# Optimization experiments

Measured on AMD Instinct MI355X. Metric: run time of the kernel, lower is better.

The kernel has to match this reference:

```python
import jax, jax.numpy as jnp
import numpy as np

B, S, D, H = 2, 2048, 1024, 16
DH = D // H
SCALE = 1.0 / float(np.sqrt(DH))


def setup_inputs() -> dict:
    key = jax.random.key(0)
    ks = jax.random.split(key, 5)
    x = jax.random.normal(ks[0], (B, S, D), dtype=jnp.float32)
    init = 0.02
    Wq = jax.random.normal(ks[1], (D, D), dtype=jnp.float32) * init
    Wk = jax.random.normal(ks[2], (D, D), dtype=jnp.float32) * init
    Wv = jax.random.normal(ks[3], (D, D), dtype=jnp.float32) * init
    Wo = jax.random.normal(ks[4], (D, D), dtype=jnp.float32) * init
    bq = jnp.zeros((D,), dtype=jnp.float32)
    bk = jnp.zeros((D,), dtype=jnp.float32)
    bv = jnp.zeros((D,), dtype=jnp.float32)
    bo = jnp.zeros((D,), dtype=jnp.float32)
    return {"x": x, "Wq": Wq, "bq": bq, "Wk": Wk, "bk": bk,
            "Wv": Wv, "bv": bv, "Wo": Wo, "bo": bo}


def reference(x, Wq, bq, Wk, bk, Wv, bv, Wo, bo):
    # torch Linear: y = x @ W.T + b  (W: [out, in])
    q = x @ Wq.T + bq  # [B,S,D]
    k = x @ Wk.T + bk
    v = x @ Wv.T + bv
    # split heads -> [B,H,S,dh]
    q = q.reshape(B, S, H, DH).transpose(0, 2, 1, 3)
    k = k.reshape(B, S, H, DH).transpose(0, 2, 1, 3)
    v = v.reshape(B, S, H, DH).transpose(0, 2, 1, 3)
    scores = jnp.einsum('bhqd,bhkd->bhqk', q, k) * SCALE  # [B,H,S,S]
    p = jax.nn.softmax(scores, axis=-1)
    o = jnp.einsum('bhqk,bhkd->bhqd', p, v)  # [B,H,S,dh]
    # faithful to original: view(B, d_model, S) then transpose(-1,-2)
    o = o.reshape(B, D, S).swapaxes(-1, -2)  # [B,S,D]
    return o @ Wo.T + bo
```

## Files before the change

kernel.cpp:

```cpp
#include <hip/hip_runtime.h>
#include <cstdint>
#include <cstddef>


typedef _Float16 h16;
typedef _Float16 h16x8 __attribute__((ext_vector_type(8)));
typedef _Float16 h16x4 __attribute__((ext_vector_type(4)));
typedef float    f32x4 __attribute__((ext_vector_type(4)));
typedef unsigned int u32x4 __attribute__((ext_vector_type(4)));

#define MFMA16 __builtin_amdgcn_mfma_f32_16x16x32_f16

#define QSCALE 0.1803368801111204f

#if __has_builtin(__builtin_amdgcn_exp2f)
#define EXP2F(x) __builtin_amdgcn_exp2f(x)
#else
#define EXP2F(x) exp2f(x)
#endif

__device__ __forceinline__ void gload_lds16(char* lds_dst, const void* gsrc) {
  __builtin_amdgcn_global_load_lds(
      (__attribute__((address_space(1))) void*)gsrc,
      (__attribute__((address_space(3))) void*)lds_dst,
      16, 0, 0);
}

__device__ __forceinline__ unsigned pk2(float lo, float hi) {
  return __builtin_bit_cast(unsigned, __builtin_amdgcn_cvt_pkrtz(lo, hi));
}

__device__ __forceinline__ void swap32(unsigned& a, unsigned& b) {
  asm("v_permlane32_swap_b32 %0, %1" : "+v"(a), "+v"(b));
}

__device__ __forceinline__ h16x8 mk8(unsigned u0, unsigned u1, unsigned u2, unsigned u3) {
  u32x4 v = {u0, u1, u2, u3};
  return __builtin_bit_cast(h16x8, v);
}


__global__ __launch_bounds__(256)
void cast_all(const float* __restrict__ x,
              const float* __restrict__ wq, const float* __restrict__ wk,
              const float* __restrict__ wv, const float* __restrict__ wo,
              h16* __restrict__ xb, h16* __restrict__ wqb, h16* __restrict__ wkb,
              h16* __restrict__ wvb, h16* __restrict__ wob) {
  const int z = blockIdx.y;
  const float* src; h16* dst; int n4;
  switch (z) {
    case 0:  src = x;  dst = xb;  n4 = 1048576; break;
    case 1:  src = wq; dst = wqb; n4 = 262144;  break;
    case 2:  src = wk; dst = wkb; n4 = 262144;  break;
    case 3:  src = wv; dst = wvb; n4 = 262144;  break;
    default: src = wo; dst = wob; n4 = 262144;  break;
  }
  int i = blockIdx.x * 256 + threadIdx.x;
  const int stride = gridDim.x * 256;
  for (; i < n4; i += stride) {
    float4 v = reinterpret_cast<const float4*>(src)[i];
    h16x4 o = { (h16)v.x, (h16)v.y, (h16)v.z, (h16)v.w };
    reinterpret_cast<h16x4*>(dst)[i] = o;
  }
}

__device__ __forceinline__ void gemm_core_128(
    const h16* __restrict__ A, const h16* __restrict__ W,
    char* lds, f32x4 (&acc)[4][4])
{
  const int tid  = threadIdx.x;
  const int lane = tid & 63;
  const int w    = tid >> 6;
  const int wr   = w >> 1, wc = w & 1;
  const int blockRow = blockIdx.y * 128;
  const int blockCol = blockIdx.x * 128;

  const int sr  = (tid >> 2) & 15;
  const int sc  = tid & 3;
  const int skc = sc ^ ((sr >> 1) & 3);

  const h16* srcA0 = A + (size_t)(blockRow + (0 * 4 + w) * 16 + sr) * 1024 + skc * 8;
  const h16* srcA1 = A + (size_t)(blockRow + (1 * 4 + w) * 16 + sr) * 1024 + skc * 8;
  const h16* srcB0 = W + (size_t)(blockCol + (0 * 4 + w) * 16 + sr) * 1024 + skc * 8;
  const h16* srcB1 = W + (size_t)(blockCol + (1 * 4 + w) * 16 + sr) * 1024 + skc * 8;

  const int dA0o = w * 1024;
  const int dA1o = 4096 + w * 1024;
  const int dB0o = 8192 + w * 1024;
  const int dB1o = 12288 + w * 1024;

  const int fr = lane & 15, fg = lane >> 4;
  const int foff = fr * 64 + ((fg ^ ((fr >> 1) & 3)) << 4);

#pragma unroll
  for (int i = 0; i < 4; ++i)
#pragma unroll
    for (int j = 0; j < 4; ++j) acc[i][j] = f32x4{0.f, 0.f, 0.f, 0.f};

  gload_lds16(lds + dA0o, srcA0);
  gload_lds16(lds + dA1o, srcA1);
  gload_lds16(lds + dB0o, srcB0);
  gload_lds16(lds + dB1o, srcB1);

  for (int ks = 0; ks < 32; ++ks) {
    char* buf = lds + (ks & 1) * 16384;
    __syncthreads();
    if (ks != 31) {
      char* nbuf = lds + ((ks & 1) ^ 1) * 16384;
      gload_lds16(nbuf + dA0o, srcA0 + (ks + 1) * 32);
      gload_lds16(nbuf + dA1o, srcA1 + (ks + 1) * 32);
      gload_lds16(nbuf + dB0o, srcB0 + (ks + 1) * 32);
      gload_lds16(nbuf + dB1o, srcB1 + (ks + 1) * 32);
    }
    char* ldsA = buf;
    char* ldsB = buf + 8192;

    h16x8 af[4], bfv[4];
#pragma unroll
    for (int t = 0; t < 4; ++t)
      af[t] = *(const h16x8*)(ldsA + (wr * 4 + t) * 1024 + foff);
#pragma unroll
    for (int t = 0; t < 4; ++t)
      bfv[t] = *(const h16x8*)(ldsB + (wc * 4 + t) * 1024 + foff);
#pragma unroll
    for (int i = 0; i < 4; ++i)
#pragma unroll
      for (int j = 0; j < 4; ++j)
        acc[i][j] = MFMA16(af[i], bfv[j], acc[i][j], 0, 0, 0);
  }
}

__global__ __launch_bounds__(256, 2)
void gemm_qkv(const h16* __restrict__ xb,
              const h16* __restrict__ wq, const h16* __restrict__ wk, const h16* __restrict__ wv,
              const float* __restrict__ bq, const float* __restrict__ bk, const float* __restrict__ bv,
              h16* __restrict__ q_, h16* __restrict__ k_, h16* __restrict__ vt_)
{
  __shared__ alignas(128) char lds[32768];
  const int z = blockIdx.z;
  const h16* W = (z == 0) ? wq : (z == 1) ? wk : wv;
  const float* bias = (z == 0) ? bq : (z == 1) ? bk : bv;

  f32x4 acc[4][4];
  gemm_core_128(xb, W, lds, acc);

  const int lane = threadIdx.x & 63;
  const int w = threadIdx.x >> 6;
  const int wr = w >> 1, wc = w & 1;
  const int fr = lane & 15, fg = lane >> 4;
  const int blockRow = blockIdx.y * 128;
  const int blockCol = blockIdx.x * 128;

  if (z == 2) {
#pragma unroll
    for (int ct = 0; ct < 4; ++ct) {
      int n = blockCol + wc * 64 + ct * 16 + fr;
      int hh = n >> 6, dd = n & 63;
      float bv_ = bias[n];
#pragma unroll
      for (int rt = 0; rt < 4; ++rt) {
        int m = blockRow + wr * 64 + rt * 16 + 4 * fg;
        int bb = m >> 11, s0 = m & 2047;
        h16x4 pack = { (h16)(acc[rt][ct][0] + bv_), (h16)(acc[rt][ct][1] + bv_),
                       (h16)(acc[rt][ct][2] + bv_), (h16)(acc[rt][ct][3] + bv_) };
        *(h16x4*)(vt_ + ((size_t)((bb * 16 + hh) * 64 + dd)) * 2048 + s0) = pack;
      }
    }
  } else {
    const float scl = (z == 0) ? QSCALE : 1.0f;
    h16* dst = (z == 0) ? q_ : k_;
#pragma unroll
    for (int ct = 0; ct < 4; ++ct) {
      int n = blockCol + wc * 64 + ct * 16 + fr;
      float bv_ = bias[n];
#pragma unroll
      for (int rt = 0; rt < 4; ++rt) {
        int m0 = blockRow + wr * 64 + rt * 16 + 4 * fg;
#pragma unroll
        for (int r = 0; r < 4; ++r)
          dst[(size_t)(m0 + r) * 1024 + n] = (h16)((acc[rt][ct][r] + bv_) * scl);
      }
    }
  }
}

__global__ __launch_bounds__(256, 2)
void gemm_out(const h16* __restrict__ yt, const h16* __restrict__ wo,
              const float* __restrict__ bo, float* __restrict__ out)
{
  __shared__ alignas(128) char lds[32768];
  f32x4 acc[4][4];
  gemm_core_128(yt, wo, lds, acc);

  const int lane = threadIdx.x & 63;
  const int w = threadIdx.x >> 6;
  const int wr = w >> 1, wc = w & 1;
  const int fr = lane & 15, fg = lane >> 4;
  const int blockRow = blockIdx.y * 128;
  const int blockCol = blockIdx.x * 128;

#pragma unroll
  for (int ct = 0; ct < 4; ++ct) {
    int n = blockCol + wc * 64 + ct * 16 + fr;
    float bv_ = bo[n];
#pragma unroll
    for (int rt = 0; rt < 4; ++rt) {
      int m0 = blockRow + wr * 64 + rt * 16 + 4 * fg;
#pragma unroll
      for (int r = 0; r < 4; ++r)
        out[(size_t)(m0 + r) * 1024 + n] = acc[rt][ct][r] + bv_;
    }
  }
}

__global__ __launch_bounds__(256, 2)
void attn_kernel(const h16* __restrict__ qb, const h16* __restrict__ kb,
                 const h16* __restrict__ vtb, h16* __restrict__ ytb)
{
  __shared__ alignas(128) char lds[32768];
  const int tid = threadIdx.x, lane = tid & 63, w = tid >> 6;
  const int fr = lane & 15, fg = lane >> 4;

  const int orig = blockIdx.x;
  const int wgid = (orig & 7) * 64 + (orig >> 3);
  const int p  = wgid & 15;
  const int hh = (wgid >> 4) & 15;
  const int b  = wgid >> 8;

  const int aq = w * 16 + fr;
  const h16* qrowA = qb + ((size_t)(b * 2048 + 32 * aq + p)) * 1024 + hh * 64;
  const h16* qrowB = qrowA + 16 * 1024;
  h16x8 qfA0 = *(const h16x8*)(qrowA + fg * 8);
  h16x8 qfA1 = *(const h16x8*)(qrowA + 32 + fg * 8);
  h16x8 qfB0 = *(const h16x8*)(qrowB + fg * 8);
  h16x8 qfB1 = *(const h16x8*)(qrowB + 32 + fg * 8);

  const int sr  = (tid >> 2) & 15;
  const int sc  = tid & 3;
  const int skc = sc ^ ((sr >> 1) & 3);
  const int rloc0 = (w >> 1) * 16 + sr;
  const int rloc1 = ((4 + w) >> 1) * 16 + sr;
  const int kc0 = (w & 1) * 32 + skc * 8;
  const int kc1 = ((4 + w) & 1) * 32 + skc * 8;

  const h16* srcK0 = kb + ((size_t)(b * 2048 + rloc0)) * 1024 + hh * 64 + kc0;
  const h16* srcK1 = kb + ((size_t)(b * 2048 + rloc1)) * 1024 + hh * 64 + kc1;
  const h16* srcV0 = vtb + ((size_t)((b * 16 + hh) * 64 + rloc0)) * 2048 + kc0;
  const h16* srcV1 = vtb + ((size_t)((b * 16 + hh) * 64 + rloc1)) * 2048 + kc1;

  const int dK0o = w * 1024, dK1o = 4096 + w * 1024;
  const int dV0o = 8192 + w * 1024, dV1o = 12288 + w * 1024;

  const int foff = fr * 64 + ((fg ^ ((fr >> 1) & 3)) << 4);
  const int sfr  = (fr & 3) | ((fr & 4) << 1) | ((fr & 8) >> 1);
  const int foffK = sfr * 64 + ((fg ^ ((sfr >> 1) & 3)) << 4);

  const h16x8 ones8 = { (h16)1.f, (h16)1.f, (h16)1.f, (h16)1.f,
                        (h16)1.f, (h16)1.f, (h16)1.f, (h16)1.f };

  f32x4 oA[4], oB[4];
#pragma unroll
  for (int i = 0; i < 4; ++i) { oA[i] = f32x4{0.f,0.f,0.f,0.f}; oB[i] = f32x4{0.f,0.f,0.f,0.f}; }
  f32x4 lA4 = f32x4{0.f,0.f,0.f,0.f}, lB4 = f32x4{0.f,0.f,0.f,0.f};

  gload_lds16(lds + dK0o, srcK0);
  gload_lds16(lds + dK1o, srcK1);
  gload_lds16(lds + dV0o, srcV0);
  gload_lds16(lds + dV1o, srcV1);

  for (int ch = 0; ch < 32; ++ch) {
    char* buf = lds + (ch & 1) * 16384;
    __syncthreads();
    if (ch != 31) {
      char* nbuf = lds + ((ch & 1) ^ 1) * 16384;
      gload_lds16(nbuf + dK0o, srcK0 + (size_t)(ch + 1) * 65536);
      gload_lds16(nbuf + dK1o, srcK1 + (size_t)(ch + 1) * 65536);
      gload_lds16(nbuf + dV0o, srcV0 + (size_t)(ch + 1) * 64);
      gload_lds16(nbuf + dV1o, srcV1 + (size_t)(ch + 1) * 64);
    }
    char* ldsK = buf;
    char* ldsV = buf + 8192;

    unsigned pA[4][2], pB[4][2];
#pragma unroll
    for (int t = 0; t < 4; ++t) {
      h16x8 kf0 = *(const h16x8*)(ldsK + (t * 2 + 0) * 1024 + foffK);
      h16x8 kf1 = *(const h16x8*)(ldsK + (t * 2 + 1) * 1024 + foffK);
      f32x4 sA = f32x4{0.f,0.f,0.f,0.f};
      f32x4 sB = f32x4{0.f,0.f,0.f,0.f};
      __builtin_amdgcn_s_setprio(1);
      sA = MFMA16(kf0, qfA0, sA, 0, 0, 0);
      sA = MFMA16(kf1, qfA1, sA, 0, 0, 0);
      sB = MFMA16(kf0, qfB0, sB, 0, 0, 0);
      sB = MFMA16(kf1, qfB1, sB, 0, 0, 0);
      __builtin_amdgcn_s_setprio(0);
      pA[t][0] = pk2(EXP2F(sA[0]), EXP2F(sA[1]));
      pA[t][1] = pk2(EXP2F(sA[2]), EXP2F(sA[3]));
      pB[t][0] = pk2(EXP2F(sB[0]), EXP2F(sB[1]));
      pB[t][1] = pk2(EXP2F(sB[2]), EXP2F(sB[3]));
    }

    swap32(pA[0][0], pA[1][0]);  swap32(pA[0][1], pA[1][1]);
    swap32(pA[2][0], pA[3][0]);  swap32(pA[2][1], pA[3][1]);
    swap32(pB[0][0], pB[1][0]);  swap32(pB[0][1], pB[1][1]);
    swap32(pB[2][0], pB[3][0]);  swap32(pB[2][1], pB[3][1]);
    h16x8 pfA0 = mk8(pA[0][0], pA[0][1], pA[1][0], pA[1][1]);
    h16x8 pfA1 = mk8(pA[2][0], pA[2][1], pA[3][0], pA[3][1]);
    h16x8 pfB0 = mk8(pB[0][0], pB[0][1], pB[1][0], pB[1][1]);
    h16x8 pfB1 = mk8(pB[2][0], pB[2][1], pB[3][0], pB[3][1]);

    __builtin_amdgcn_s_setprio(1);
    lA4 = MFMA16(pfA0, ones8, lA4, 0, 0, 0);
    lA4 = MFMA16(pfA1, ones8, lA4, 0, 0, 0);
    lB4 = MFMA16(pfB0, ones8, lB4, 0, 0, 0);
    lB4 = MFMA16(pfB1, ones8, lB4, 0, 0, 0);
#pragma unroll
    for (int dt = 0; dt < 4; ++dt) {
      h16x8 vf0 = *(const h16x8*)(ldsV + (dt * 2 + 0) * 1024 + foff);
      h16x8 vf1 = *(const h16x8*)(ldsV + (dt * 2 + 1) * 1024 + foff);
      oA[dt] = MFMA16(pfA0, vf0, oA[dt], 0, 0, 0);
      oA[dt] = MFMA16(pfA1, vf1, oA[dt], 0, 0, 0);
      oB[dt] = MFMA16(pfB0, vf0, oB[dt], 0, 0, 0);
      oB[dt] = MFMA16(pfB1, vf1, oB[dt], 0, 0, 0);
    }
    __builtin_amdgcn_s_setprio(0);
  }

  f32x4 iA4, iB4;
#pragma unroll
  for (int r = 0; r < 4; ++r) { iA4[r] = 1.0f / lA4[r]; iB4[r] = 1.0f / lB4[r]; }

#pragma unroll
  for (int dt = 0; dt < 4; ++dt) {
    int row = dt * 16 + fr;
    size_t colb = (size_t)(hh * 64 + w * 16 + fg * 4);
    h16x4 sA4 = { (h16)(oA[dt][0] * iA4[0]), (h16)(oA[dt][1] * iA4[1]),
                  (h16)(oA[dt][2] * iA4[2]), (h16)(oA[dt][3] * iA4[3]) };
    h16x4 sB4 = { (h16)(oB[dt][0] * iB4[0]), (h16)(oB[dt][1] * iB4[1]),
                  (h16)(oB[dt][2] * iB4[2]), (h16)(oB[dt][3] * iB4[3]) };
    *(h16x4*)(ytb + ((size_t)(b * 2048 + p * 64 + row)) * 1024 + colb) = sA4;
    *(h16x4*)(ytb + ((size_t)(b * 2048 + (p + 16) * 64 + row)) * 1024 + colb) = sB4;
  }
}

extern "C" void kernel_launch(void* const* d_in, const int* in_sizes, int n_in,
                              void* d_out, int out_size, void* d_ws, size_t ws_size,
                              hipStream_t stream) {
  const float* x  = (const float*)d_in[0];
  const float* Wq = (const float*)d_in[1];
  const float* bq = (const float*)d_in[2];
  const float* Wk = (const float*)d_in[3];
  const float* bk = (const float*)d_in[4];
  const float* Wv = (const float*)d_in[5];
  const float* bv = (const float*)d_in[6];
  const float* Wo = (const float*)d_in[7];
  const float* bo = (const float*)d_in[8];

  char* ws = (char*)d_ws;
  h16* xb  = (h16*)(ws);
  h16* wqb = (h16*)(ws + (size_t)(8  << 20));
  h16* wkb = (h16*)(ws + (size_t)(10 << 20));
  h16* wvb = (h16*)(ws + (size_t)(12 << 20));
  h16* wob = (h16*)(ws + (size_t)(14 << 20));
  h16* q_  = (h16*)(ws + (size_t)(16 << 20));
  h16* k_  = (h16*)(ws + (size_t)(24 << 20));
  h16* vt_ = (h16*)(ws + (size_t)(32 << 20));
  h16* yt_ = (h16*)(ws + (size_t)(40 << 20));

  cast_all<<<dim3(512, 5), 256, 0, stream>>>(x, Wq, Wk, Wv, Wo, xb, wqb, wkb, wvb, wob);
  gemm_qkv<<<dim3(8, 32, 3), 256, 0, stream>>>(xb, wqb, wkb, wvb, bq, bk, bv, q_, k_, vt_);
  attn_kernel<<<512, 256, 0, stream>>>(q_, k_, vt_, yt_);
  gemm_out<<<dim3(8, 32, 1), 256, 0, stream>>>(yt_, wob, bo, (float*)d_out);
}
```

Measured before the change: 107.5 us.

## Double query rows per attention workgroup to reuse K/V tiles, halving grid

Each attention workgroup now handles four query sub-tiles instead of two, so every K/V chunk staged in LDS feeds twice as many MFMAs. The grid drops from 512 to 256 blocks, and launch bounds are relaxed to one block per CU to make room for the larger register footprint. This cuts K/V global-to-LDS traffic per unit of work. In exchange, 256 blocks may leave part of the GPU idle and occupancy falls, so there is less latency hiding.

New measurement: 118.2 us. 1.1x slower.

```diff
diff --git a/kernel.cpp b/kernel.cpp
--- a/kernel.cpp
+++ b/kernel.cpp
@@ -213,7 +213,7 @@
   }
 }
 
-__global__ __launch_bounds__(256, 2)
+__global__ __launch_bounds__(256, 1)
 void attn_kernel(const h16* __restrict__ qb, const h16* __restrict__ kb,
                  const h16* __restrict__ vtb, h16* __restrict__ ytb)
 {
@@ -222,18 +222,19 @@
   const int fr = lane & 15, fg = lane >> 4;
 
   const int orig = blockIdx.x;
-  const int wgid = (orig & 7) * 64 + (orig >> 3);
-  const int p  = wgid & 15;
-  const int hh = (wgid >> 4) & 15;
-  const int b  = wgid >> 8;
+  const int wgid = (orig & 7) * 32 + (orig >> 3);
+  const int p  = wgid & 7;
+  const int hh = (wgid >> 3) & 15;
+  const int b  = wgid >> 7;
 
   const int aq = w * 16 + fr;
-  const h16* qrowA = qb + ((size_t)(b * 2048 + 32 * aq + p)) * 1024 + hh * 64;
-  const h16* qrowB = qrowA + 16 * 1024;
-  h16x8 qfA0 = *(const h16x8*)(qrowA + fg * 8);
-  h16x8 qfA1 = *(const h16x8*)(qrowA + 32 + fg * 8);
-  h16x8 qfB0 = *(const h16x8*)(qrowB + fg * 8);
-  h16x8 qfB1 = *(const h16x8*)(qrowB + 32 + fg * 8);
+  const h16* qrow0 = qb + ((size_t)(b * 2048 + 32 * aq + p)) * 1024 + hh * 64;
+  h16x8 qf[4][2];
+#pragma unroll
+  for (int X = 0; X < 4; ++X) {
+    qf[X][0] = *(const h16x8*)(qrow0 + (size_t)(8 * X) * 1024 + fg * 8);
+    qf[X][1] = *(const h16x8*)(qrow0 + (size_t)(8 * X) * 1024 + 32 + fg * 8);
+  }
 
   const int sr  = (tid >> 2) & 15;
   const int sc  = tid & 3;
@@ -258,10 +259,14 @@
   const h16x8 ones8 = { (h16)1.f, (h16)1.f, (h16)1.f, (h16)1.f,
                         (h16)1.f, (h16)1.f, (h16)1.f, (h16)1.f };
 
-  f32x4 oA[4], oB[4];
-#pragma unroll
-  for (int i = 0; i < 4; ++i) { oA[i] = f32x4{0.f,0.f,0.f,0.f}; oB[i] = f32x4{0.f,0.f,0.f,0.f}; }
-  f32x4 lA4 = f32x4{0.f,0.f,0.f,0.f}, lB4 = f32x4{0.f,0.f,0.f,0.f};
+  f32x4 o[4][4];
+  f32x4 l4[4];
+#pragma unroll
+  for (int X = 0; X < 4; ++X) {
+    l4[X] = f32x4{0.f,0.f,0.f,0.f};
+#pragma unroll
+    for (int dt = 0; dt < 4; ++dt) o[X][dt] = f32x4{0.f,0.f,0.f,0.f};
+  }
 
   gload_lds16(lds + dK0o, srcK0);
   gload_lds16(lds + dK1o, srcK1);
@@ -281,65 +286,71 @@
     char* ldsK = buf;
     char* ldsV = buf + 8192;
 
-    unsigned pA[4][2], pB[4][2];
+    unsigned pp[4][4][2];
 #pragma unroll
     for (int t = 0; t < 4; ++t) {
       h16x8 kf0 = *(const h16x8*)(ldsK + (t * 2 + 0) * 1024 + foffK);
       h16x8 kf1 = *(const h16x8*)(ldsK + (t * 2 + 1) * 1024 + foffK);
-      f32x4 sA = f32x4{0.f,0.f,0.f,0.f};
-      f32x4 sB = f32x4{0.f,0.f,0.f,0.f};
+      f32x4 s[4];
       __builtin_amdgcn_s_setprio(1);
-      sA = MFMA16(kf0, qfA0, sA, 0, 0, 0);
-      sA = MFMA16(kf1, qfA1, sA, 0, 0, 0);
-      sB = MFMA16(kf0, qfB0, sB, 0, 0, 0);
-      sB = MFMA16(kf1, qfB1, sB, 0, 0, 0);
+#pragma unroll
+      for (int X = 0; X < 4; ++X) {
+        s[X] = f32x4{0.f,0.f,0.f,0.f};
+        s[X] = MFMA16(kf0, qf[X][0], s[X], 0, 0, 0);
+        s[X] = MFMA16(kf1, qf[X][1], s[X], 0, 0, 0);
+      }
       __builtin_amdgcn_s_setprio(0);
-      pA[t][0] = pk2(EXP2F(sA[0]), EXP2F(sA[1]));
-      pA[t][1] = pk2(EXP2F(sA[2]), EXP2F(sA[3]));
-      pB[t][0] = pk2(EXP2F(sB[0]), EXP2F(sB[1]));
-      pB[t][1] = pk2(EXP2F(sB[2]), EXP2F(sB[3]));
-    }
-
-    swap32(pA[0][0], pA[1][0]);  swap32(pA[0][1], pA[1][1]);
-    swap32(pA[2][0], pA[3][0]);  swap32(pA[2][1], pA[3][1]);
-    swap32(pB[0][0], pB[1][0]);  swap32(pB[0][1], pB[1][1]);
-    swap32(pB[2][0], pB[3][0]);  swap32(pB[2][1], pB[3][1]);
-    h16x8 pfA0 = mk8(pA[0][0], pA[0][1], pA[1][0], pA[1][1]);
-    h16x8 pfA1 = mk8(pA[2][0], pA[2][1], pA[3][0], pA[3][1]);
-    h16x8 pfB0 = mk8(pB[0][0], pB[0][1], pB[1][0], pB[1][1]);
-    h16x8 pfB1 = mk8(pB[2][0], pB[2][1], pB[3][0], pB[3][1]);
+#pragma unroll
+      for (int X = 0; X < 4; ++X) {
+        pp[X][t][0] = pk2(EXP2F(s[X][0]), EXP2F(s[X][1]));
+        pp[X][t][1] = pk2(EXP2F(s[X][2]), EXP2F(s[X][3]));
+      }
+    }
+
+    h16x8 pf[4][2];
+#pragma unroll
+    for (int X = 0; X < 4; ++X) {
+      swap32(pp[X][0][0], pp[X][1][0]);  swap32(pp[X][0][1], pp[X][1][1]);
+      swap32(pp[X][2][0], pp[X][3][0]);  swap32(pp[X][2][1], pp[X][3][1]);
+      pf[X][0] = mk8(pp[X][0][0], pp[X][0][1], pp[X][1][0], pp[X][1][1]);
+      pf[X][1] = mk8(pp[X][2][0], pp[X][2][1], pp[X][3][0], pp[X][3][1]);
+    }
 
     __builtin_amdgcn_s_setprio(1);
-    lA4 = MFMA16(pfA0, ones8, lA4, 0, 0, 0);
-    lA4 = MFMA16(pfA1, ones8, lA4, 0, 0, 0);
-    lB4 = MFMA16(pfB0, ones8, lB4, 0, 0, 0);
-    lB4 = MFMA16(pfB1, ones8, lB4, 0, 0, 0);
+#pragma unroll
+    for (int X = 0; X < 4; ++X) {
+      l4[X] = MFMA16(pf[X][0], ones8, l4[X], 0, 0, 0);
+      l4[X] = MFMA16(pf[X][1], ones8, l4[X], 0, 0, 0);
+    }
 #pragma unroll
     for (int dt = 0; dt < 4; ++dt) {
       h16x8 vf0 = *(const h16x8*)(ldsV + (dt * 2 + 0) * 1024 + foff);
       h16x8 vf1 = *(const h16x8*)(ldsV + (dt * 2 + 1) * 1024 + foff);
-      oA[dt] = MFMA16(pfA0, vf0, oA[dt], 0, 0, 0);
-      oA[dt] = MFMA16(pfA1, vf1, oA[dt], 0, 0, 0);
-      oB[dt] = MFMA16(pfB0, vf0, oB[dt], 0, 0, 0);
-      oB[dt] = MFMA16(pfB1, vf1, oB[dt], 0, 0, 0);
+#pragma unroll
+      for (int X = 0; X < 4; ++X) {
+        o[X][dt] = MFMA16(pf[X][0], vf0, o[X][dt], 0, 0, 0);
+        o[X][dt] = MFMA16(pf[X][1], vf1, o[X][dt], 0, 0, 0);
+      }
     }
     __builtin_amdgcn_s_setprio(0);
   }
 
-  f32x4 iA4, iB4;
-#pragma unroll
-  for (int r = 0; r < 4; ++r) { iA4[r] = 1.0f / lA4[r]; iB4[r] = 1.0f / lB4[r]; }
-
-#pragma unroll
-  for (int dt = 0; dt < 4; ++dt) {
-    int row = dt * 16 + fr;
-    size_t colb = (size_t)(hh * 64 + w * 16 + fg * 4);
-    h16x4 sA4 = { (h16)(oA[dt][0] * iA4[0]), (h16)(oA[dt][1] * iA4[1]),
-                  (h16)(oA[dt][2] * iA4[2]), (h16)(oA[dt][3] * iA4[3]) };
-    h16x4 sB4 = { (h16)(oB[dt][0] * iB4[0]), (h16)(oB[dt][1] * iB4[1]),
-                  (h16)(oB[dt][2] * iB4[2]), (h16)(oB[dt][3] * iB4[3]) };
-    *(h16x4*)(ytb + ((size_t)(b * 2048 + p * 64 + row)) * 1024 + colb) = sA4;
-    *(h16x4*)(ytb + ((size_t)(b * 2048 + (p + 16) * 64 + row)) * 1024 + colb) = sB4;
+  f32x4 i4[4];
+#pragma unroll
+  for (int X = 0; X < 4; ++X)
+#pragma unroll
+    for (int r = 0; r < 4; ++r) i4[X][r] = 1.0f / l4[X][r];
+
+#pragma unroll
+  for (int X = 0; X < 4; ++X) {
+#pragma unroll
+    for (int dt = 0; dt < 4; ++dt) {
+      int row = dt * 16 + fr;
+      size_t colb = (size_t)(hh * 64 + w * 16 + fg * 4);
+      h16x4 s4 = { (h16)(o[X][dt][0] * i4[X][0]), (h16)(o[X][dt][1] * i4[X][1]),
+                   (h16)(o[X][dt][2] * i4[X][2]), (h16)(o[X][dt][3] * i4[X][3]) };
+      *(h16x4*)(ytb + ((size_t)(b * 2048 + (p + 8 * X) * 64 + row)) * 1024 + colb) = s4;
+    }
   }
 }
 
@@ -369,6 +380,6 @@
 
   cast_all<<<dim3(512, 5), 256, 0, stream>>>(x, Wq, Wk, Wv, Wo, xb, wqb, wkb, wvb, wob);
   gemm_qkv<<<dim3(8, 32, 3), 256, 0, stream>>>(xb, wqb, wkb, wvb, bq, bk, bv, q_, k_, vt_);
-  attn_kernel<<<512, 256, 0, stream>>>(q_, k_, vt_, yt_);
+  attn_kernel<<<256, 256, 0, stream>>>(q_, k_, vt_, yt_);
   gemm_out<<<dim3(8, 32, 1), 256, 0, stream>>>(yt_, wob, bo, (float*)d_out);
 }
```
